# Kernel optimization log

Measured on AMD Instinct MI355X. Metric: run time of the kernel, lower is better.

Reference implementation:

```python
import jax, jax.numpy as jnp
import numpy as np

H = 8        # num_heads
DK = 128     # head_k_dim
DV = 128     # head_v_dim
HID = 1024   # hidden_size
CHUNK = 64   # chunk size for chunked linear attention
EPS = 1e-5


def setup_inputs() -> dict:
    key = jax.random.key(0)
    ks = jax.random.split(key, 16)
    s = 0.02
    inp = {
        "hidden_states": jax.random.normal(ks[0], (2, 8192, HID), dtype=jnp.float32),
        "Wq": jax.random.normal(ks[1], (HID, HID), dtype=jnp.float32) * s,
        "Wk": jax.random.normal(ks[2], (HID, HID), dtype=jnp.float32) * s,
        "Wv": jax.random.normal(ks[3], (HID, HID), dtype=jnp.float32) * s,
        "fmq_w1": jax.random.normal(ks[4], (DK, DK), dtype=jnp.float32) * s,
        "fmq_b1": jnp.zeros((DK,), dtype=jnp.float32),
        "fmq_w2": jax.random.normal(ks[5], (DK, DK), dtype=jnp.float32) * s,
        "fmq_b2": jnp.zeros((DK,), dtype=jnp.float32),
        "fmk_w1": jax.random.normal(ks[6], (DK, DK), dtype=jnp.float32) * s,
        "fmk_b1": jnp.zeros((DK,), dtype=jnp.float32),
        "fmk_w2": jax.random.normal(ks[7], (DK, DK), dtype=jnp.float32) * s,
        "fmk_b2": jnp.zeros((DK,), dtype=jnp.float32),
        "rms_w": jnp.ones((DV,), dtype=jnp.float32),
        "Wo": jax.random.normal(ks[8], (HID, HID), dtype=jnp.float32) * s,
    }
    return inp


def reference(hidden_states, Wq, Wk, Wv, fmq_w1, fmq_b1, fmq_w2, fmq_b2,
              fmk_w1, fmk_b1, fmk_w2, fmk_b2, rms_w, Wo):
    B, T, _ = hidden_states.shape
    scale = DK ** -0.5

    # projections (torch Linear: x @ W.T), split heads -> [B,T,H,D]
    q = (hidden_states @ Wq.T).reshape(B, T, H, DK)
    k = (hidden_states @ Wk.T).reshape(B, T, H, DK)
    v = (hidden_states @ Wv.T).reshape(B, T, H, DV)

    # Hadamard feature maps: l1(x) * l2(x)
    q = (q @ fmq_w1.T + fmq_b1) * (q @ fmq_w2.T + fmq_b2)
    k = (k @ fmk_w1.T + fmk_b1) * (k @ fmk_w2.T + fmk_b2)

    q = q * scale

    # chunked causal linear attention: o_t = q_t @ sum_{s<=t} k_s v_s^T
    N = T // CHUNK
    qc = q.reshape(B, N, CHUNK, H, DK)
    kc = k.reshape(B, N, CHUNK, H, DK)
    vc = v.reshape(B, N, CHUNK, H, DV)

    # per-chunk KV outer-product sums, exclusive prefix over chunks
    kv = jnp.einsum('bnchk,bnchv->bnhkv', kc, vc)
    S = jnp.cumsum(kv, axis=1) - kv  # state entering each chunk

    o_inter = jnp.einsum('bnchk,bnhkv->bnchv', qc, S)

    # intra-chunk causal part
    A = jnp.einsum('bnihk,bnjhk->bnhij', qc, kc)
    causal = jnp.tril(jnp.ones((CHUNK, CHUNK), dtype=bool))
    A = jnp.where(causal, A, 0.0)
    o_intra = jnp.einsum('bnhij,bnjhv->bnihv', A, vc)

    o = (o_inter + o_intra).reshape(B, T, H, DV)

    # RMSNorm over head_v_dim with affine weight
    o = o * jax.lax.rsqrt(jnp.mean(o * o, axis=-1, keepdims=True) + EPS) * rms_w

    o = o.reshape(B, T, H * DV) @ Wo.T
    return o
```

## Files before the change

### kernel.cpp

```cpp
#include <hip/hip_runtime.h>


typedef __bf16 bf16x8 __attribute__((ext_vector_type(8)));
typedef float  f32x4  __attribute__((ext_vector_type(4)));

__device__ __forceinline__ float bf2f(unsigned short u) {
  union { unsigned int i; float f; } v; v.i = ((unsigned int)u) << 16; return v.f;
}
__device__ __forceinline__ unsigned short f2bf(float f) {
  union { float f; unsigned int i; } v; v.f = f;
  return (unsigned short)((v.i + 0x8000u) >> 16);
}
__device__ __forceinline__ unsigned int pk2(float a, float b) {
  union { float f; unsigned int i; } x, y; x.f = a; y.f = b;
  return ((x.i + 0x8000u) >> 16) | ((y.i + 0x8000u) & 0xFFFF0000u);
}
__device__ __forceinline__ f32x4 mfma16(bf16x8 a, bf16x8 b, f32x4 c) {
  return __builtin_amdgcn_mfma_f32_16x16x32_bf16(a, b, c, 0, 0, 0);
}
__device__ __forceinline__ void gl_lds16(const unsigned short* g, unsigned short* l) {
  __builtin_amdgcn_global_load_lds((const __attribute__((address_space(1))) void*)g,
                                   (__attribute__((address_space(3))) void*)l, 16, 0, 0);
}

__global__ void __launch_bounds__(256)
cvt_kernel(const float* __restrict__ s, unsigned short* __restrict__ d, int n4) {
  const int i = blockIdx.x * 256 + threadIdx.x;
  if (i >= n4) return;
  const float4 f = ((const float4*)s)[i];
  uint2 o; o.x = pk2(f.x, f.y); o.y = pk2(f.z, f.w);
  ((uint2*)d)[i] = o;
}

__global__ void __launch_bounds__(256)
qkv_gemm(const unsigned short* __restrict__ Xb,
         const unsigned short* __restrict__ Wqb, const unsigned short* __restrict__ Wkb,
         const unsigned short* __restrict__ Wvb,
         unsigned short* __restrict__ Q, unsigned short* __restrict__ Kf,
         unsigned short* __restrict__ VT) {
  constexpr int K = 1024;
  __shared__ unsigned short As[128 * 32];
  __shared__ unsigned short Bs[128 * 32];
  const int tid = threadIdx.x;
  const int bx = blockIdx.x;
  const int rowBase = blockIdx.y * 128;
  const int sel = bx >> 3;
  const int colBase = (bx & 7) * 128;
  const unsigned short* Bw = (sel == 0) ? Wqb : ((sel == 1) ? Wkb : Wvb);

  const int lane = tid & 63, wid = tid >> 6;
  const int lq = lane & 15, quad = lane >> 4;
  const int wm = (wid >> 1) * 64, wn = (wid & 1) * 64;

  const int srow = wid * 32 + (lane >> 2);
  const int scol = (lane & 3) * 8;
  const unsigned short* gA = Xb + (size_t)(rowBase + srow) * K + scol;
  const unsigned short* gB = Bw + (size_t)(colBase + srow) * K + scol;
  unsigned short* lA0 = As + wid * 1024;
  unsigned short* lA1 = As + wid * 1024 + 512;
  unsigned short* lB0 = Bs + wid * 1024;
  unsigned short* lB1 = Bs + wid * 1024 + 512;

  f32x4 acc[4][4] = {};
  for (int kt = 0; kt < K / 32; ++kt) {
    __syncthreads();
    gl_lds16(gA + kt * 32, lA0);
    gl_lds16(gA + kt * 32 + 16 * K, lA1);
    gl_lds16(gB + kt * 32, lB0);
    gl_lds16(gB + kt * 32 + 16 * K, lB1);
    __syncthreads();
    bf16x8 af[4], bfr[4];
#pragma unroll
    for (int i = 0; i < 4; ++i)
      af[i] = *(const bf16x8*)(As + (wm + i * 16 + lq) * 32 + quad * 8);
#pragma unroll
    for (int j = 0; j < 4; ++j)
      bfr[j] = *(const bf16x8*)(Bs + (wn + j * 16 + lq) * 32 + quad * 8);
#pragma unroll
    for (int i = 0; i < 4; ++i)
#pragma unroll
      for (int j = 0; j < 4; ++j) acc[i][j] = mfma16(af[i], bfr[j], acc[i][j]);
  }
  if (sel < 2) {
    unsigned short* C = (sel == 0) ? Q : Kf;
#pragma unroll
    for (int i = 0; i < 4; ++i)
#pragma unroll
      for (int j = 0; j < 4; ++j) {
        const int col = colBase + wn + j * 16 + lq;
#pragma unroll
        for (int r = 0; r < 4; ++r) {
          const int row = rowBase + wm + i * 16 + quad * 4 + r;
          C[(size_t)row * 1024 + col] = f2bf(acc[i][j][r]);
        }
      }
  } else {
#pragma unroll
    for (int i = 0; i < 4; ++i)
#pragma unroll
      for (int j = 0; j < 4; ++j) {
        const int col = colBase + wn + j * 16 + lq;
        const int h = col >> 7, dv = col & 127;
        const int row0 = rowBase + wm + i * 16 + quad * 4;
        const int b = row0 >> 13, tl = row0 & 8191;
        ushort4 t4;
        t4.x = f2bf(acc[i][j][0]); t4.y = f2bf(acc[i][j][1]);
        t4.z = f2bf(acc[i][j][2]); t4.w = f2bf(acc[i][j][3]);
        *(ushort4*)(VT + (((size_t)(b * 8 + h) * 128 + dv) << 13) + tl) = t4;
      }
  }
}

__global__ void __launch_bounds__(256)
out_gemm(const unsigned short* __restrict__ A, const unsigned short* __restrict__ Bw,
         float* __restrict__ C) {
  constexpr int K = 1024;
  __shared__ unsigned short As[128 * 32];
  __shared__ unsigned short Bs[128 * 32];
  const int tid = threadIdx.x;
  const int rowBase = blockIdx.y * 128;
  const int colBase = blockIdx.x * 128;
  const int lane = tid & 63, wid = tid >> 6;
  const int lq = lane & 15, quad = lane >> 4;
  const int wm = (wid >> 1) * 64, wn = (wid & 1) * 64;

  const int srow = wid * 32 + (lane >> 2);
  const int scol = (lane & 3) * 8;
  const unsigned short* gA = A + (size_t)(rowBase + srow) * K + scol;
  const unsigned short* gB = Bw + (size_t)(colBase + srow) * K + scol;
  unsigned short* lA0 = As + wid * 1024;
  unsigned short* lA1 = As + wid * 1024 + 512;
  unsigned short* lB0 = Bs + wid * 1024;
  unsigned short* lB1 = Bs + wid * 1024 + 512;

  f32x4 acc[4][4] = {};
  for (int kt = 0; kt < K / 32; ++kt) {
    __syncthreads();
    gl_lds16(gA + kt * 32, lA0);
    gl_lds16(gA + kt * 32 + 16 * K, lA1);
    gl_lds16(gB + kt * 32, lB0);
    gl_lds16(gB + kt * 32 + 16 * K, lB1);
    __syncthreads();
    bf16x8 af[4], bfr[4];
#pragma unroll
    for (int i = 0; i < 4; ++i)
      af[i] = *(const bf16x8*)(As + (wm + i * 16 + lq) * 32 + quad * 8);
#pragma unroll
    for (int j = 0; j < 4; ++j)
      bfr[j] = *(const bf16x8*)(Bs + (wn + j * 16 + lq) * 32 + quad * 8);
#pragma unroll
    for (int i = 0; i < 4; ++i)
#pragma unroll
      for (int j = 0; j < 4; ++j) acc[i][j] = mfma16(af[i], bfr[j], acc[i][j]);
  }
#pragma unroll
  for (int i = 0; i < 4; ++i)
#pragma unroll
    for (int j = 0; j < 4; ++j) {
      const int col = colBase + wn + j * 16 + lq;
#pragma unroll
      for (int r = 0; r < 4; ++r) {
        const int row = rowBase + wm + i * 16 + quad * 4 + r;
        C[(size_t)row * 1024 + col] = acc[i][j][r];
      }
    }
}

__global__ void __launch_bounds__(256)
fm_kernel(unsigned short* __restrict__ buf,
          const unsigned short* __restrict__ w1b, const float* __restrict__ b1,
          const unsigned short* __restrict__ w2b, const float* __restrict__ b2,
          float scale) {
  __shared__ unsigned short Aq[64 * 136];
  const int tid = threadIdx.x;
  const int t0 = blockIdx.x * 64;
  const int h = blockIdx.y, hc = h * 128;
#pragma unroll
  for (int it = 0; it < 4; ++it) {
    const int p = tid + it * 256;
    const int row = p >> 4, c8 = (p & 15) * 8;
    *(uint4*)(Aq + row * 136 + c8) =
        *(const uint4*)(buf + (size_t)(t0 + row) * 1024 + hc + c8);
  }
  __syncthreads();
  const int lane = tid & 63, wid = tid >> 6, lq = lane & 15, quad = lane >> 4;
  const int wn = wid * 32;
  f32x4 a1[4][2] = {}, a2[4][2] = {};
#pragma unroll
  for (int ks = 0; ks < 4; ++ks) {
    bf16x8 af[4];
#pragma unroll
    for (int i = 0; i < 4; ++i)
      af[i] = *(const bf16x8*)(Aq + (i * 16 + lq) * 136 + ks * 32 + quad * 8);
#pragma unroll
    for (int j = 0; j < 2; ++j) {
      const int nr = wn + j * 16 + lq;
      bf16x8 w1f = *(const bf16x8*)(w1b + nr * 128 + ks * 32 + quad * 8);
      bf16x8 w2f = *(const bf16x8*)(w2b + nr * 128 + ks * 32 + quad * 8);
#pragma unroll
      for (int i = 0; i < 4; ++i) {
        a1[i][j] = mfma16(af[i], w1f, a1[i][j]);
        a2[i][j] = mfma16(af[i], w2f, a2[i][j]);
      }
    }
  }
#pragma unroll
  for (int j = 0; j < 2; ++j) {
    const int col = wn + j * 16 + lq;
    const float bb1 = b1[col], bb2 = b2[col];
#pragma unroll
    for (int i = 0; i < 4; ++i)
#pragma unroll
      for (int r = 0; r < 4; ++r) {
        const float v = (a1[i][j][r] + bb1) * (a2[i][j][r] + bb2) * scale;
        buf[(size_t)(t0 + i * 16 + quad * 4 + r) * 1024 + hc + col] = f2bf(v);
      }
  }
}

__global__ void __launch_bounds__(256)
kv_kernel(const unsigned short* __restrict__ Kf, const unsigned short* __restrict__ VT,
          unsigned short* __restrict__ KV) {
  __shared__ unsigned short Kt[128 * 72];
  __shared__ unsigned short Vt[128 * 72];
  const int tid = threadIdx.x;
  const int n = blockIdx.x, bh = blockIdx.y;
  const int b = bh >> 3, h = bh & 7;
  const int t0g = b * 8192 + n * 64;
  const int tl0 = n * 64;
#pragma unroll
  for (int it = 0; it < 4; ++it) {
    const int p = tid + it * 256;
    const int d = p >> 3, c8 = (p & 7) * 8;
    *(uint4*)(Vt + d * 72 + c8) =
        *(const uint4*)(VT + (((size_t)bh * 128 + d) << 13) + tl0 + c8);
    const int tok = p >> 4, c8k = (p & 15) * 8;
    const unsigned short* src = Kf + (size_t)(t0g + tok) * 1024 + h * 128 + c8k;
    ushort4 k0 = *(const ushort4*)(src);
    ushort4 k1 = *(const ushort4*)(src + 4);
    Kt[(c8k + 0) * 72 + tok] = k0.x; Kt[(c8k + 1) * 72 + tok] = k0.y;
    Kt[(c8k + 2) * 72 + tok] = k0.z; Kt[(c8k + 3) * 72 + tok] = k0.w;
    Kt[(c8k + 4) * 72 + tok] = k1.x; Kt[(c8k + 5) * 72 + tok] = k1.y;
    Kt[(c8k + 6) * 72 + tok] = k1.z; Kt[(c8k + 7) * 72 + tok] = k1.w;
  }
  __syncthreads();
  const int lane = tid & 63, wid = tid >> 6, lq = lane & 15, quad = lane >> 4;
  const int wm = (wid >> 1) * 64, wn = (wid & 1) * 64;
  f32x4 acc[4][4] = {};
#pragma unroll
  for (int ks = 0; ks < 2; ++ks) {
    bf16x8 af[4], bfr[4];
#pragma unroll
    for (int i = 0; i < 4; ++i)
      af[i] = *(const bf16x8*)(Vt + (wm + i * 16 + lq) * 72 + ks * 32 + quad * 8);
#pragma unroll
    for (int j = 0; j < 4; ++j)
      bfr[j] = *(const bf16x8*)(Kt + (wn + j * 16 + lq) * 72 + ks * 32 + quad * 8);
#pragma unroll
    for (int i = 0; i < 4; ++i)
#pragma unroll
      for (int j = 0; j < 4; ++j) acc[i][j] = mfma16(af[i], bfr[j], acc[i][j]);
  }
  const size_t base = ((size_t)bh * 128 + n) * 16384;
#pragma unroll
  for (int i = 0; i < 4; ++i)
#pragma unroll
    for (int j = 0; j < 4; ++j)
#pragma unroll
      for (int r = 0; r < 4; ++r)
        KV[base + (size_t)(wm + i * 16 + quad * 4 + r) * 128 + wn + j * 16 + lq] =
            f2bf(acc[i][j][r]);
}

__global__ void __launch_bounds__(256)
cumsum_kernel(unsigned short* __restrict__ KV) {
  const int idx = blockIdx.x * 256 + threadIdx.x;
  const int bh = idx >> 14, e = idx & 16383;
  unsigned short* p = KV + (size_t)bh * (128 * 16384) + e;
  float run = 0.f;
  for (int n = 0; n < 128; ++n) {
    const float x = bf2f(*p);
    *p = f2bf(run);
    run += x;
    p += 16384;
  }
}

__global__ void __launch_bounds__(256)
attn_kernel(const unsigned short* __restrict__ Q, const unsigned short* __restrict__ Kf,
            const unsigned short* __restrict__ VT, const unsigned short* __restrict__ S,
            const float* __restrict__ rmsw, unsigned short* __restrict__ O) {
  __shared__ uint4 smem4[3968];
  unsigned short* sm = (unsigned short*)smem4;
  unsigned short* SQ = sm;
  unsigned short* KS = sm + 8704;
  unsigned short* VTl = sm + 17920;
  unsigned short* AL = sm + 27136;
  float* OL = (float*)sm;
  float* RED = (float*)AL;
  float* SCL = RED + 256;

  const int tid = threadIdx.x;
  const int n = blockIdx.x, bh = blockIdx.y;
  const int b = bh >> 3, h = bh & 7;
  const int t0g = b * 8192 + n * 64;
  const int tl0 = n * 64;
  const int lane = tid & 63, wid = tid >> 6, lq = lane & 15, quad = lane >> 4;

#pragma unroll
  for (int it = 0; it < 4; ++it) {
    const int p = tid + it * 256;
    const int row = p >> 4, c8 = (p & 15) * 8;
    *(uint4*)(SQ + row * 136 + c8) =
        *(const uint4*)(Q + (size_t)(t0g + row) * 1024 + h * 128 + c8);
    *(uint4*)(KS + row * 136 + c8) =
        *(const uint4*)(Kf + (size_t)(t0g + row) * 1024 + h * 128 + c8);
    const int d = p >> 3, c8b = (p & 7) * 8;
    *(uint4*)(VTl + d * 72 + c8b) =
        *(const uint4*)(VT + (((size_t)bh * 128 + d) << 13) + tl0 + c8b);
  }
  __syncthreads();

  {
    f32x4 aa[4] = {};
#pragma unroll
    for (int ks = 0; ks < 4; ++ks) {
      bf16x8 kf = *(const bf16x8*)(KS + (wid * 16 + lq) * 136 + ks * 32 + quad * 8);
#pragma unroll
      for (int i = 0; i < 4; ++i) {
        bf16x8 qf = *(const bf16x8*)(SQ + (i * 16 + lq) * 136 + ks * 32 + quad * 8);
        aa[i] = mfma16(qf, kf, aa[i]);
      }
    }
#pragma unroll
    for (int i = 0; i < 4; ++i)
#pragma unroll
      for (int r = 0; r < 4; ++r) {
        const int qp = i * 16 + quad * 4 + r, kp = wid * 16 + lq;
        AL[qp * 72 + kp] = f2bf(kp <= qp ? aa[i][r] : 0.f);
      }
  }
  __syncthreads();

  const size_t sbase = ((size_t)bh * 128 + n) * 16384;
#pragma unroll
  for (int it = 0; it < 4; ++it) {
    const int p = tid + it * 256;
    const int dv = p >> 3, c8 = (p & 7) * 8;
    *(uint4*)(KS + dv * 72 + c8) = *(const uint4*)(S + sbase + (size_t)dv * 128 + c8);
  }
  __syncthreads();

  f32x4 oa[4][2] = {};
#pragma unroll
  for (int ks = 0; ks < 2; ++ks) {
    bf16x8 bv[2], sf[2];
#pragma unroll
    for (int j = 0; j < 2; ++j) {
      bv[j] = *(const bf16x8*)(VTl + (wid * 32 + j * 16 + lq) * 72 + ks * 32 + quad * 8);
      sf[j] = *(const bf16x8*)(KS + (wid * 32 + j * 16 + lq) * 72 + ks * 32 + quad * 8);
    }
#pragma unroll
    for (int i = 0; i < 4; ++i) {
      bf16x8 af = *(const bf16x8*)(AL + (i * 16 + lq) * 72 + ks * 32 + quad * 8);
      bf16x8 qf = *(const bf16x8*)(SQ + (i * 16 + lq) * 136 + ks * 32 + quad * 8);
#pragma unroll
      for (int j = 0; j < 2; ++j) {
        oa[i][j] = mfma16(af, bv[j], oa[i][j]);
        oa[i][j] = mfma16(qf, sf[j], oa[i][j]);
      }
    }
  }
  __syncthreads();

#pragma unroll
  for (int it = 0; it < 4; ++it) {
    const int p = tid + it * 256;
    const int dv = p >> 3, c8 = (p & 7) * 8;
    *(uint4*)(KS + dv * 72 + c8) =
        *(const uint4*)(S + sbase + (size_t)dv * 128 + 64 + c8);
  }
  __syncthreads();

#pragma unroll
  for (int ks = 0; ks < 2; ++ks) {
    bf16x8 sf[2];
#pragma unroll
    for (int j = 0; j < 2; ++j)
      sf[j] = *(const bf16x8*)(KS + (wid * 32 + j * 16 + lq) * 72 + ks * 32 + quad * 8);
#pragma unroll
    for (int i = 0; i < 4; ++i) {
      bf16x8 qf = *(const bf16x8*)(SQ + (i * 16 + lq) * 136 + (ks + 2) * 32 + quad * 8);
#pragma unroll
      for (int j = 0; j < 2; ++j) oa[i][j] = mfma16(qf, sf[j], oa[i][j]);
    }
  }
  __syncthreads();

#pragma unroll
  for (int i = 0; i < 4; ++i)
#pragma unroll
    for (int j = 0; j < 2; ++j)
#pragma unroll
      for (int r = 0; r < 4; ++r)
        OL[(i * 16 + quad * 4 + r) * 132 + wid * 32 + j * 16 + lq] = oa[i][j][r];
  __syncthreads();

  {
    const int r = tid >> 2, part = tid & 3;
    const float* pr = OL + r * 132 + part * 32;
    float s = 0.f;
#pragma unroll
    for (int c = 0; c < 32; ++c) { const float v = pr[c]; s += v * v; }
    RED[r * 4 + part] = s;
  }
  __syncthreads();
  if (tid < 64) {
    const float ms = (RED[tid * 4] + RED[tid * 4 + 1] + RED[tid * 4 + 2] + RED[tid * 4 + 3]) *
                     (1.f / 128.f);
    SCL[tid] = rsqrtf(ms + 1e-5f);
  }
  __syncthreads();

#pragma unroll
  for (int it = 0; it < 4; ++it) {
    const int r = (tid >> 4) + it * 16;
    const int c8 = (tid & 15) * 8;
    const float sc = SCL[r];
    unsigned short us[8];
#pragma unroll
    for (int e = 0; e < 8; ++e)
      us[e] = f2bf(OL[r * 132 + c8 + e] * sc * rmsw[c8 + e]);
    uint4 pk;
    pk.x = (unsigned int)us[0] | ((unsigned int)us[1] << 16);
    pk.y = (unsigned int)us[2] | ((unsigned int)us[3] << 16);
    pk.z = (unsigned int)us[4] | ((unsigned int)us[5] << 16);
    pk.w = (unsigned int)us[6] | ((unsigned int)us[7] << 16);
    *(uint4*)(O + (size_t)(t0g + r) * 1024 + h * 128 + c8) = pk;
  }
}

extern "C" void kernel_launch(void* const* d_in, const int* in_sizes, int n_in,
                              void* d_out, int out_size, void* d_ws, size_t ws_size,
                              hipStream_t stream) {
  const float* X    = (const float*)d_in[0];
  const float* Wq   = (const float*)d_in[1];
  const float* Wk   = (const float*)d_in[2];
  const float* Wv   = (const float*)d_in[3];
  const float* fq1  = (const float*)d_in[4];
  const float* fqb1 = (const float*)d_in[5];
  const float* fq2  = (const float*)d_in[6];
  const float* fqb2 = (const float*)d_in[7];
  const float* fk1  = (const float*)d_in[8];
  const float* fkb1 = (const float*)d_in[9];
  const float* fk2  = (const float*)d_in[10];
  const float* fkb2 = (const float*)d_in[11];
  const float* rmsw = (const float*)d_in[12];
  const float* Wo   = (const float*)d_in[13];

  const size_t MB = 1u << 20;
  char* ws = (char*)d_ws;
  unsigned short* Q    = (unsigned short*)(ws);
  unsigned short* Kf   = (unsigned short*)(ws + 32 * MB);
  unsigned short* VT   = (unsigned short*)(ws + 64 * MB);
  unsigned short* KV   = (unsigned short*)(ws + 96 * MB);
  unsigned short* Xb   = KV;
  unsigned short* Wqb  = (unsigned short*)(ws + 160 * MB);
  unsigned short* Wkb  = (unsigned short*)(ws + 162 * MB);
  unsigned short* Wvb  = (unsigned short*)(ws + 164 * MB);
  unsigned short* Wob  = (unsigned short*)(ws + 166 * MB);
  unsigned short* fq1b = (unsigned short*)(ws + 168 * MB);
  unsigned short* fq2b = fq1b + 16384;
  unsigned short* fk1b = fq1b + 32768;
  unsigned short* fk2b = fq1b + 49152;
  unsigned short* O    = Q;

  cvt_kernel<<<1024, 256, 0, stream>>>(Wq, Wqb, 262144);
  cvt_kernel<<<1024, 256, 0, stream>>>(Wk, Wkb, 262144);
  cvt_kernel<<<1024, 256, 0, stream>>>(Wv, Wvb, 262144);
  cvt_kernel<<<1024, 256, 0, stream>>>(Wo, Wob, 262144);
  cvt_kernel<<<16, 256, 0, stream>>>(fq1, fq1b, 4096);
  cvt_kernel<<<16, 256, 0, stream>>>(fq2, fq2b, 4096);
  cvt_kernel<<<16, 256, 0, stream>>>(fk1, fk1b, 4096);
  cvt_kernel<<<16, 256, 0, stream>>>(fk2, fk2b, 4096);
  cvt_kernel<<<16384, 256, 0, stream>>>(X, Xb, 4194304);

  qkv_gemm<<<dim3(24, 128), 256, 0, stream>>>(Xb, Wqb, Wkb, Wvb, Q, Kf, VT);
  fm_kernel<<<dim3(256, 8), 256, 0, stream>>>(Q, fq1b, fqb1, fq2b, fqb2,
                                              0.08838834764831843f);
  fm_kernel<<<dim3(256, 8), 256, 0, stream>>>(Kf, fk1b, fkb1, fk2b, fkb2, 1.0f);
  kv_kernel<<<dim3(128, 16), 256, 0, stream>>>(Kf, VT, KV);
  cumsum_kernel<<<1024, 256, 0, stream>>>(KV);
  attn_kernel<<<dim3(128, 16), 256, 0, stream>>>(Q, Kf, VT, KV, rmsw, O);
  out_gemm<<<dim3(8, 128), 256, 0, stream>>>(O, Wob, (float*)d_out);
}
```

Before: 486.4 us.

## Fuse Hadamard feature maps into QKV GEMM epilogue and batch weight conversions

The Hadamard feature-map computation for Q and K now runs as an epilogue of the QKV projection GEMM. Each 128x128 output tile (exactly one head's 128 dims) is staged in LDS as bf16 and multiplied by the two 128x128 feature-map weights. This removes two separate kernel launches and a full write and re-read of Q and K through global memory. Separately, the eight weight-conversion launches become two batched launches. In exchange, the GEMM kernel needs about 34KB more LDS and holds 32 extra f32x4 accumulators per thread, which may lower occupancy of the main GEMM.

```diff
diff --git a/kernel.cpp b/kernel.cpp
--- a/kernel.cpp
+++ b/kernel.cpp
@@ -31,16 +31,36 @@
   uint2 o; o.x = pk2(f.x, f.y); o.y = pk2(f.z, f.w);
   ((uint2*)d)[i] = o;
 }
+__global__ void __launch_bounds__(256)
+cvt4_kernel(const float* __restrict__ s0, const float* __restrict__ s1,
+            const float* __restrict__ s2, const float* __restrict__ s3,
+            unsigned short* __restrict__ d0, unsigned short* __restrict__ d1,
+            unsigned short* __restrict__ d2, unsigned short* __restrict__ d3,
+            int n4) {
+  const int w = blockIdx.y;
+  const float* s = (w == 0) ? s0 : (w == 1) ? s1 : (w == 2) ? s2 : s3;
+  unsigned short* d = (w == 0) ? d0 : (w == 1) ? d1 : (w == 2) ? d2 : d3;
+  const int i = blockIdx.x * 256 + threadIdx.x;
+  if (i >= n4) return;
+  const float4 f = ((const float4*)s)[i];
+  uint2 o; o.x = pk2(f.x, f.y); o.y = pk2(f.z, f.w);
+  ((uint2*)d)[i] = o;
+}
 
 __global__ void __launch_bounds__(256)
 qkv_gemm(const unsigned short* __restrict__ Xb,
          const unsigned short* __restrict__ Wqb, const unsigned short* __restrict__ Wkb,
          const unsigned short* __restrict__ Wvb,
+         const unsigned short* __restrict__ fq1b, const unsigned short* __restrict__ fq2b,
+         const unsigned short* __restrict__ fk1b, const unsigned short* __restrict__ fk2b,
+         const float* __restrict__ fqb1, const float* __restrict__ fqb2,
+         const float* __restrict__ fkb1, const float* __restrict__ fkb2,
          unsigned short* __restrict__ Q, unsigned short* __restrict__ Kf,
          unsigned short* __restrict__ VT) {
   constexpr int K = 1024;
   __shared__ unsigned short As[128 * 32];
   __shared__ unsigned short Bs[128 * 32];
+  __shared__ unsigned short Qs[128 * 136];
   const int tid = threadIdx.x;
   const int bx = blockIdx.x;
   const int rowBase = blockIdx.y * 128;
@@ -81,20 +101,8 @@
 #pragma unroll
       for (int j = 0; j < 4; ++j) acc[i][j] = mfma16(af[i], bfr[j], acc[i][j]);
   }
-  if (sel < 2) {
-    unsigned short* C = (sel == 0) ? Q : Kf;
-#pragma unroll
-    for (int i = 0; i < 4; ++i)
-#pragma unroll
-      for (int j = 0; j < 4; ++j) {
-        const int col = colBase + wn + j * 16 + lq;
-#pragma unroll
-        for (int r = 0; r < 4; ++r) {
-          const int row = rowBase + wm + i * 16 + quad * 4 + r;
-          C[(size_t)row * 1024 + col] = f2bf(acc[i][j][r]);
-        }
-      }
-  } else {
+
+  if (sel == 2) {
 #pragma unroll
     for (int i = 0; i < 4; ++i)
 #pragma unroll
@@ -107,6 +115,57 @@
         t4.x = f2bf(acc[i][j][0]); t4.y = f2bf(acc[i][j][1]);
         t4.z = f2bf(acc[i][j][2]); t4.w = f2bf(acc[i][j][3]);
         *(ushort4*)(VT + (((size_t)(b * 8 + h) * 128 + dv) << 13) + tl) = t4;
+      }
+    return;
+  }
+
+#pragma unroll
+  for (int i = 0; i < 4; ++i)
+#pragma unroll
+    for (int j = 0; j < 4; ++j)
+#pragma unroll
+      for (int r = 0; r < 4; ++r)
+        Qs[(wm + i * 16 + quad * 4 + r) * 136 + wn + j * 16 + lq] =
+            f2bf(acc[i][j][r]);
+  __syncthreads();
+
+  const unsigned short* w1 = (sel == 0) ? fq1b : fk1b;
+  const unsigned short* w2 = (sel == 0) ? fq2b : fk2b;
+  const float* b1 = (sel == 0) ? fqb1 : fkb1;
+  const float* b2 = (sel == 0) ? fqb2 : fkb2;
+  const float scale = (sel == 0) ? 0.08838834764831843f : 1.0f;
+  unsigned short* C = (sel == 0) ? Q : Kf;
+
+  f32x4 a1[4][4] = {}, a2[4][4] = {};
+#pragma unroll
+  for (int ks = 0; ks < 4; ++ks) {
+    bf16x8 af[4];
+#pragma unroll
+    for (int i = 0; i < 4; ++i)
+      af[i] = *(const bf16x8*)(Qs + (wm + i * 16 + lq) * 136 + ks * 32 + quad * 8);
+#pragma unroll
+    for (int j = 0; j < 4; ++j) {
+      const int nr = wn + j * 16 + lq;
+      bf16x8 w1f = *(const bf16x8*)(w1 + nr * 128 + ks * 32 + quad * 8);
+      bf16x8 w2f = *(const bf16x8*)(w2 + nr * 128 + ks * 32 + quad * 8);
+#pragma unroll
+      for (int i = 0; i < 4; ++i) {
+        a1[i][j] = mfma16(af[i], w1f, a1[i][j]);
+        a2[i][j] = mfma16(af[i], w2f, a2[i][j]);
+      }
+    }
+  }
+#pragma unroll
+  for (int j = 0; j < 4; ++j) {
+    const int col = wn + j * 16 + lq;
+    const float bb1 = b1[col], bb2 = b2[col];
+#pragma unroll
+    for (int i = 0; i < 4; ++i)
+#pragma unroll
+      for (int r = 0; r < 4; ++r) {
+        const int row = rowBase + wm + i * 16 + quad * 4 + r;
+        const float v = (a1[i][j][r] + bb1) * (a2[i][j][r] + bb2) * scale;
+        C[(size_t)row * 1024 + colBase + col] = f2bf(v);
       }
   }
 }
@@ -164,58 +223,6 @@
         C[(size_t)row * 1024 + col] = acc[i][j][r];
       }
     }
-}
-
-__global__ void __launch_bounds__(256)
-fm_kernel(unsigned short* __restrict__ buf,
-          const unsigned short* __restrict__ w1b, const float* __restrict__ b1,
-          const unsigned short* __restrict__ w2b, const float* __restrict__ b2,
-          float scale) {
-  __shared__ unsigned short Aq[64 * 136];
-  const int tid = threadIdx.x;
-  const int t0 = blockIdx.x * 64;
-  const int h = blockIdx.y, hc = h * 128;
-#pragma unroll
-  for (int it = 0; it < 4; ++it) {
-    const int p = tid + it * 256;
-    const int row = p >> 4, c8 = (p & 15) * 8;
-    *(uint4*)(Aq + row * 136 + c8) =
-        *(const uint4*)(buf + (size_t)(t0 + row) * 1024 + hc + c8);
-  }
-  __syncthreads();
-  const int lane = tid & 63, wid = tid >> 6, lq = lane & 15, quad = lane >> 4;
-  const int wn = wid * 32;
-  f32x4 a1[4][2] = {}, a2[4][2] = {};
-#pragma unroll
-  for (int ks = 0; ks < 4; ++ks) {
-    bf16x8 af[4];
-#pragma unroll
-    for (int i = 0; i < 4; ++i)
-      af[i] = *(const bf16x8*)(Aq + (i * 16 + lq) * 136 + ks * 32 + quad * 8);
-#pragma unroll
-    for (int j = 0; j < 2; ++j) {
-      const int nr = wn + j * 16 + lq;
-      bf16x8 w1f = *(const bf16x8*)(w1b + nr * 128 + ks * 32 + quad * 8);
-      bf16x8 w2f = *(const bf16x8*)(w2b + nr * 128 + ks * 32 + quad * 8);
-#pragma unroll
-      for (int i = 0; i < 4; ++i) {
-        a1[i][j] = mfma16(af[i], w1f, a1[i][j]);
-        a2[i][j] = mfma16(af[i], w2f, a2[i][j]);
-      }
-    }
-  }
-#pragma unroll
-  for (int j = 0; j < 2; ++j) {
-    const int col = wn + j * 16 + lq;
-    const float bb1 = b1[col], bb2 = b2[col];
-#pragma unroll
-    for (int i = 0; i < 4; ++i)
-#pragma unroll
-      for (int r = 0; r < 4; ++r) {
-        const float v = (a1[i][j][r] + bb1) * (a2[i][j][r] + bb2) * scale;
-        buf[(size_t)(t0 + i * 16 + quad * 4 + r) * 1024 + hc + col] = f2bf(v);
-      }
-  }
 }
 
 __global__ void __launch_bounds__(256)
@@ -475,20 +482,16 @@
   unsigned short* fk2b = fq1b + 49152;
   unsigned short* O    = Q;
 
-  cvt_kernel<<<1024, 256, 0, stream>>>(Wq, Wqb, 262144);
-  cvt_kernel<<<1024, 256, 0, stream>>>(Wk, Wkb, 262144);
-  cvt_kernel<<<1024, 256, 0, stream>>>(Wv, Wvb, 262144);
-  cvt_kernel<<<1024, 256, 0, stream>>>(Wo, Wob, 262144);
-  cvt_kernel<<<16, 256, 0, stream>>>(fq1, fq1b, 4096);
-  cvt_kernel<<<16, 256, 0, stream>>>(fq2, fq2b, 4096);
-  cvt_kernel<<<16, 256, 0, stream>>>(fk1, fk1b, 4096);
-  cvt_kernel<<<16, 256, 0, stream>>>(fk2, fk2b, 4096);
+  cvt4_kernel<<<dim3(1024, 4), 256, 0, stream>>>(Wq, Wk, Wv, Wo,
+                                                 Wqb, Wkb, Wvb, Wob, 262144);
+  cvt4_kernel<<<dim3(16, 4), 256, 0, stream>>>(fq1, fq2, fk1, fk2,
+                                               fq1b, fq2b, fk1b, fk2b, 4096);
   cvt_kernel<<<16384, 256, 0, stream>>>(X, Xb, 4194304);
 
-  qkv_gemm<<<dim3(24, 128), 256, 0, stream>>>(Xb, Wqb, Wkb, Wvb, Q, Kf, VT);
-  fm_kernel<<<dim3(256, 8), 256, 0, stream>>>(Q, fq1b, fqb1, fq2b, fqb2,
-                                              0.08838834764831843f);
-  fm_kernel<<<dim3(256, 8), 256, 0, stream>>>(Kf, fk1b, fkb1, fk2b, fkb2, 1.0f);
+  qkv_gemm<<<dim3(24, 128), 256, 0, stream>>>(Xb, Wqb, Wkb, Wvb,
+                                              fq1b, fq2b, fk1b, fk2b,
+                                              fqb1, fqb2, fkb1, fkb2,
+                                              Q, Kf, VT);
   kv_kernel<<<dim3(128, 16), 256, 0, stream>>>(Kf, VT, KV);
   cumsum_kernel<<<1024, 256, 0, stream>>>(KV);
   attn_kernel<<<dim3(128, 16), 256, 0, stream>>>(Q, Kf, VT, KV, rmsw, O);
```

Measured after the change: 558.0 us. 14.7% more time.
